# Optimization experiments

Hardware: AMD Instinct MI355X
Metric: run time of the kernel (lower is better)

Reference implementation:

```python
import jax, jax.numpy as jnp
import numpy as np

N = 50000  # num nodes


def _gcn_layer(x, W, b, src, dst, dinv):
    # PyG GCNConv: transform first, then normalized neighbor aggregation
    h = x @ W                                   # [N, out]
    norm = dinv[src] * dinv[dst]                # [E]
    msg = h[src] * norm[:, None]                # gather + scale, [E, out]
    agg = jax.ops.segment_sum(msg, dst, num_segments=N)
    agg = agg + h * (dinv * dinv)[:, None]      # self-loop term (weight 1)
    return agg + b


def setup_inputs() -> dict:
    key = jax.random.key(0)
    ks = jax.random.split(key, 9)
    x = jax.random.normal(ks[0], (N, 256), dtype=jnp.float32)
    edge_index = jax.random.randint(ks[1], (2, 800000), 0, N, dtype=jnp.int64)
    def lin(kw, kb, fan_in, fan_out):
        s = 1.0 / np.sqrt(fan_in)
        W = jax.random.uniform(kw, (fan_in, fan_out), jnp.float32, -s, s)
        b = jax.random.uniform(kb, (fan_out,), jnp.float32, -s, s)
        return W, b
    W0, b0 = lin(ks[2], ks[3], 256, 128)
    W1, b1 = lin(ks[4], ks[5], 128, 128)
    W2, b2 = lin(ks[6], ks[7], 128, 64)
    return {"x": x, "edge_index": edge_index,
            "W0": W0, "b0": b0, "W1": W1, "b1": b1, "W2": W2, "b2": b2}


def reference(x, edge_index, W0, b0, W1, b1, W2, b2):
    src, dst = edge_index[0], edge_index[1]
    # degree with implicit self loops (edge weights = 1)
    deg = jax.ops.segment_sum(jnp.ones_like(dst, dtype=x.dtype), dst,
                              num_segments=N) + 1.0
    dinv = jax.lax.rsqrt(deg)
    h = jax.nn.relu(_gcn_layer(x, W0, b0, src, dst, dinv))
    h = jax.nn.relu(_gcn_layer(h, W1, b1, src, dst, dinv))
    out = _gcn_layer(h, W2, b2, src, dst, dinv)  # no relu on final layer
    return out
```

## Files before the change

### kernel.cpp

```cpp
#include <hip/hip_runtime.h>

#define NNODES 50000
#define NEDGES 800000
#define CHUNK 3125

typedef __attribute__((ext_vector_type(8))) short short8;
typedef __attribute__((ext_vector_type(4))) float floatx4;
typedef __attribute__((ext_vector_type(8))) _Float16 f16x8;

__device__ __forceinline__ void async16(const void* g, void* l) {
    __builtin_amdgcn_global_load_lds(
        (const __attribute__((address_space(1))) unsigned int*)g,
        (__attribute__((address_space(3))) unsigned int*)l, 16, 0, 0);
}

__device__ __forceinline__ void split_bf16(float v, short& hi, short& lo) {
    unsigned u = __float_as_uint(v);
    unsigned hu = u & 0xffff0000u;
    hi = (short)(hu >> 16);
    float r = v - __uint_as_float(hu);
    lo = (short)(__float_as_uint(r) >> 16);
}


#define PREP_WBLK 224
#define PREP_SBLK 6250
#define PREP_TOT  (PREP_WBLK + PREP_SBLK + 256)

__global__ __launch_bounds__(256) void k_prep(
    const float* __restrict__ W0, short* __restrict__ W0h, short* __restrict__ W0l,
    const float* __restrict__ W1, short* __restrict__ W1h, short* __restrict__ W1l,
    const float* __restrict__ W2, short* __restrict__ W2h, short* __restrict__ W2l,
    const float* __restrict__ x, short* __restrict__ xh, short* __restrict__ xl,
    const int* __restrict__ dst, int* __restrict__ hist2d) {
    int b = blockIdx.x, t = threadIdx.x;
    if (b < PREP_WBLK) {
        int id = b * 256 + t;
        const float* W; short *Wh, *Wl; int K, F;
        if (id < 32768) { W = W0; Wh = W0h; Wl = W0l; K = 256; F = 128; }
        else if (id < 49152) { id -= 32768; W = W1; Wh = W1h; Wl = W1l; K = 128; F = 128; }
        else if (id < 57344) { id -= 49152; W = W2; Wh = W2h; Wl = W2l; K = 128; F = 64; }
        else return;
        int f = id / K, k = id - f * K;
        short h, l;
        split_bf16(W[(size_t)k * F + f], h, l);
        Wh[id] = h;
        Wl[id] = l;
    } else if (b < PREP_WBLK + PREP_SBLK) {
        int i = (b - PREP_WBLK) * 256 + t;
        float4 v0 = ((const float4*)x)[i * 2];
        float4 v1 = ((const float4*)x)[i * 2 + 1];
        float va[8] = {v0.x, v0.y, v0.z, v0.w, v1.x, v1.y, v1.z, v1.w};
        short8 h8, l8;
#pragma unroll
        for (int j = 0; j < 8; j++) {
            short h, l;
            split_bf16(va[j], h, l);
            h8[j] = h; l8[j] = l;
        }
        *(short8*)&xh[i * 8] = h8;
        *(short8*)&xl[i * 8] = l8;
    } else {
        __shared__ int h[256];
        int bb = b - PREP_WBLK - PREP_SBLK;
        h[t] = 0;
        __syncthreads();
        int e0 = bb * CHUNK;
#pragma unroll
        for (int k = 0; k < 13; k++) {
            int o = k * 256 + t;
            if (o < CHUNK) atomicAdd(&h[dst[e0 + o] >> 8], 1);
        }
        __syncthreads();
        hist2d[bb * 256 + t] = h[t];
    }
}

__global__ __launch_bounds__(256) void k_p2(const int* __restrict__ src,
                                            const int* __restrict__ dst,
                                            const int* __restrict__ hist2d,
                                            unsigned* __restrict__ buck) {
    __shared__ int ex[256], cur[256];
    int t = threadIdx.x, b = blockIdx.x;
    int tot = 0, pre = 0;
    for (int bb = 0; bb < 256; bb++) {
        int v = hist2d[bb * 256 + t];
        tot += v;
        pre += (bb < b) ? v : 0;
    }
    ex[t] = tot;
    __syncthreads();
    for (int o = 1; o < 256; o <<= 1) {
        int xx = (t >= o) ? ex[t - o] : 0;
        __syncthreads();
        ex[t] += xx;
        __syncthreads();
    }
    cur[t] = (ex[t] - tot) + pre;
    __syncthreads();
    int e0 = b * CHUNK;
#pragma unroll
    for (int k = 0; k < 13; k++) {
        int o = k * 256 + t;
        if (o < CHUNK) {
            int s = src[e0 + o], d = dst[e0 + o];
            int p = atomicAdd(&cur[d >> 8], 1);
            buck[p] = (unsigned)s | ((unsigned)(d & 255) << 16);
        }
    }
}

__global__ __launch_bounds__(256) void k_p3(const unsigned* __restrict__ buck,
                                            const int* __restrict__ hist2d,
                                            int* __restrict__ rowptr,
                                            float* __restrict__ dinv,
                                            int* __restrict__ ssrc) {
    __shared__ int ex[256], cur[256], h[256], sS0[1], sS[1];
    int t = threadIdx.x, b = blockIdx.x;
    int tot = 0;
    for (int bb = 0; bb < 256; bb++) tot += hist2d[bb * 256 + t];
    ex[t] = tot;
    __syncthreads();
    for (int o = 1; o < 256; o <<= 1) {
        int xx = (t >= o) ? ex[t - o] : 0;
        __syncthreads();
        ex[t] += xx;
        __syncthreads();
    }
    if (t == b) { sS0[0] = ex[t] - tot; sS[0] = tot; }
    h[t] = 0;
    __syncthreads();
    int s0 = sS0[0], S = sS[0];
    for (int i = t; i < S; i += 256)
        atomicAdd(&h[(buck[s0 + i] >> 16) & 255], 1);
    __syncthreads();
    int v = h[t];
    ex[t] = v;
    __syncthreads();
    for (int o = 1; o < 256; o <<= 1) {
        int xx = (t >= o) ? ex[t - o] : 0;
        __syncthreads();
        ex[t] += xx;
        __syncthreads();
    }
    int excl = ex[t] - v;
    int n = b * 256 + t;
    if (n < NNODES) {
        rowptr[n] = s0 + excl;
        dinv[n] = rsqrtf((float)v + 1.0f);
    }
    if (b == 0 && t == 0) rowptr[NNODES] = NEDGES;
    cur[t] = excl;
    __syncthreads();
    for (int i = t; i < S; i += 256) {
        unsigned pk = buck[s0 + i];
        int dl = (pk >> 16) & 255;
        int p = atomicAdd(&cur[dl], 1);
        ssrc[s0 + p] = (int)(pk & 0xFFFFu);
    }
}


template <int BN>
__global__ __launch_bounds__(256) void k_gemm2(
    const short* __restrict__ Ah, const short* __restrict__ Al,
    const short* __restrict__ Bh, const short* __restrict__ Bl,
    const float* __restrict__ dinv, _Float16* __restrict__ g16,
    int M, int K) {
    constexpr int BM = 64, BK = 64;
    constexpr int NT = BN / 16;
    __shared__ __align__(16) short sAh[BM * BK], sAl[BM * BK];
    __shared__ __align__(16) short sBh[BN * BK], sBl[BN * BK];

    const int tid = threadIdx.x, lane = tid & 63, w = tid >> 6;
    const int row0 = blockIdx.x * BM;
    const int lr = lane >> 3;
    const int lz = lane & 7;
    const int swz = (lz ^ lr) * 8;
    const int fr = lane & 15, fq = lane >> 4;

    floatx4 acc[NT] = {};

    for (int k0 = 0; k0 < K; k0 += BK) {
#pragma unroll
        for (int jj = 0; jj < 2; jj++) {
            int j = w * 2 + jj;
            int grow = row0 + j * 8 + lr;
            if (grow >= M) grow = M - 1;
            size_t go = (size_t)grow * K + k0 + swz;
            async16(&Ah[go], &sAh[j * 8 * BK + lane * 8]);
            async16(&Al[go], &sAl[j * 8 * BK + lane * 8]);
        }
#pragma unroll
        for (int jj = 0; jj < BN / 32; jj++) {
            int j = w * (BN / 32) + jj;
            size_t go = (size_t)(j * 8 + lr) * K + k0 + swz;
            async16(&Bh[go], &sBh[j * 8 * BK + lane * 8]);
            async16(&Bl[go], &sBl[j * 8 * BK + lane * 8]);
        }
        __syncthreads();

#pragma unroll
        for (int ks = 0; ks < 2; ks++) {
            int R = w * 16 + fr;
            int ca = ((ks * 4 + fq) ^ (R & 7)) * 8;
            short8 ah = *(const short8*)&sAh[R * BK + ca];
            short8 al = *(const short8*)&sAl[R * BK + ca];
#pragma unroll
            for (int nt = 0; nt < NT; nt++) {
                int n = nt * 16 + fr;
                int cb = ((ks * 4 + fq) ^ (n & 7)) * 8;
                short8 bh = *(const short8*)&sBh[n * BK + cb];
                short8 bl = *(const short8*)&sBl[n * BK + cb];
                acc[nt] = __builtin_amdgcn_mfma_f32_16x16x32_bf16(ah, bh, acc[nt], 0, 0, 0);
                acc[nt] = __builtin_amdgcn_mfma_f32_16x16x32_bf16(ah, bl, acc[nt], 0, 0, 0);
                acc[nt] = __builtin_amdgcn_mfma_f32_16x16x32_bf16(al, bh, acc[nt], 0, 0, 0);
            }
        }
        __syncthreads();
    }

#pragma unroll
    for (int rr = 0; rr < 4; rr++) {
        int grow = row0 + w * 16 + fq * 4 + rr;
        if (grow < M) {
            float dv = dinv[grow];
#pragma unroll
            for (int nt = 0; nt < NT; nt++)
                g16[(size_t)grow * BN + nt * 16 + fr] =
                    (_Float16)(acc[nt][rr] * dv);
        }
    }
}


template <int F>
__global__ __launch_bounds__(256) void k_agg(const _Float16* __restrict__ g,
                                             const int* __restrict__ ssrc,
                                             const int* __restrict__ rowptr,
                                             const float* __restrict__ dinv,
                                             const float* __restrict__ bias,
                                             float* __restrict__ outf,
                                             short* __restrict__ oh,
                                             short* __restrict__ ol,
                                             int relu, int writebf) {
    constexpr int F8 = F / 8;
    int gid = blockIdx.x * 256 + threadIdx.x;
    int n = gid / F8;
    if (n >= NNODES) return;
    int c8 = gid - n * F8;
    const f16x8* gp = (const f16x8*)g;

    f16x8 sv = gp[(size_t)n * F8 + c8];
    float a0[8], a1[8], a2[8], a3[8];
#pragma unroll
    for (int j = 0; j < 8; j++) {
        a0[j] = (float)sv[j];
        a1[j] = 0.f; a2[j] = 0.f; a3[j] = 0.f;
    }
    int e0 = rowptr[n], e1 = rowptr[n + 1];
    int e = e0;
    for (; e + 4 <= e1; e += 4) {
        int s0 = ssrc[e], s1 = ssrc[e + 1], s2 = ssrc[e + 2], s3 = ssrc[e + 3];
        f16x8 v0 = gp[(size_t)s0 * F8 + c8];
        f16x8 v1 = gp[(size_t)s1 * F8 + c8];
        f16x8 v2 = gp[(size_t)s2 * F8 + c8];
        f16x8 v3 = gp[(size_t)s3 * F8 + c8];
#pragma unroll
        for (int j = 0; j < 8; j++) {
            a0[j] += (float)v0[j];
            a1[j] += (float)v1[j];
            a2[j] += (float)v2[j];
            a3[j] += (float)v3[j];
        }
    }
    for (; e < e1; e++) {
        int s = ssrc[e];
        f16x8 v = gp[(size_t)s * F8 + c8];
#pragma unroll
        for (int j = 0; j < 8; j++) a0[j] += (float)v[j];
    }
    float dv = dinv[n];
    float o[8];
#pragma unroll
    for (int j = 0; j < 8; j++) {
        float s = (a0[j] + a1[j]) + (a2[j] + a3[j]);
        o[j] = s * dv + bias[c8 * 8 + j];
        if (relu) o[j] = fmaxf(o[j], 0.f);
    }
    if (writebf) {
        short8 h8, l8;
#pragma unroll
        for (int j = 0; j < 8; j++) {
            short h, l;
            split_bf16(o[j], h, l);
            h8[j] = h; l8[j] = l;
        }
        *(short8*)&oh[(size_t)n * F + c8 * 8] = h8;
        *(short8*)&ol[(size_t)n * F + c8 * 8] = l8;
    } else {
        *(float4*)&outf[(size_t)n * F + c8 * 8] =
            make_float4(o[0], o[1], o[2], o[3]);
        *(float4*)&outf[(size_t)n * F + c8 * 8 + 4] =
            make_float4(o[4], o[5], o[6], o[7]);
    }
}


static inline size_t align256(size_t x) { return (x + 255) & ~(size_t)255; }

extern "C" void kernel_launch(void* const* d_in, const int* in_sizes, int n_in,
                              void* d_out, int out_size, void* d_ws, size_t ws_size,
                              hipStream_t stream) {
    const float* x  = (const float*)d_in[0];
    const int*   ei = (const int*)d_in[1];
    const float* W0 = (const float*)d_in[2];
    const float* b0 = (const float*)d_in[3];
    const float* W1 = (const float*)d_in[4];
    const float* b1 = (const float*)d_in[5];
    const float* W2 = (const float*)d_in[6];
    const float* b2 = (const float*)d_in[7];
    float* out = (float*)d_out;

    const int* src = ei;
    const int* dst = ei + NEDGES;

    char* w = (char*)d_ws;
    size_t off = 0;
    float* dinv    = (float*)(w + off); off = align256(off + NNODES * 4);
    int* rowptr    = (int*)(w + off);   off = align256(off + (NNODES + 1) * 4);
    int* hist2d    = (int*)(w + off);   off = align256(off + 256 * 256 * 4);
    unsigned* buck = (unsigned*)(w + off); off = align256(off + (size_t)NEDGES * 4);
    int* ssrc      = (int*)(w + off);   off = align256(off + (size_t)NEDGES * 4);
    short* W0h     = (short*)(w + off); off = align256(off + 256 * 128 * 2);
    short* W0l     = (short*)(w + off); off = align256(off + 256 * 128 * 2);
    short* W1h     = (short*)(w + off); off = align256(off + 128 * 128 * 2);
    short* W1l     = (short*)(w + off); off = align256(off + 128 * 128 * 2);
    short* W2h     = (short*)(w + off); off = align256(off + 128 * 64 * 2);
    short* W2l     = (short*)(w + off); off = align256(off + 128 * 64 * 2);
    short* xh      = (short*)(w + off); off = align256(off + (size_t)NNODES * 256 * 2);
    short* xl      = (short*)(w + off); off = align256(off + (size_t)NNODES * 256 * 2);
    short* ph      = (short*)(w + off); off = align256(off + (size_t)NNODES * 128 * 2);
    short* pl      = (short*)(w + off); off = align256(off + (size_t)NNODES * 128 * 2);
    _Float16* g16  = (_Float16*)(w + off); off = align256(off + (size_t)NNODES * 128 * 2);

    k_prep<<<PREP_TOT, 256, 0, stream>>>(W0, W0h, W0l, W1, W1h, W1l,
                                         W2, W2h, W2l, x, xh, xl, dst, hist2d);
    k_p2<<<256, 256, 0, stream>>>(src, dst, hist2d, buck);
    k_p3<<<256, 256, 0, stream>>>(buck, hist2d, rowptr, dinv, ssrc);

    const int MB = (NNODES + 63) / 64;
    const int AB128 = (NNODES * 16 + 255) / 256;
    const int AB64  = (NNODES * 8 + 255) / 256;

    k_gemm2<128><<<MB, 256, 0, stream>>>(xh, xl, W0h, W0l, dinv, g16, NNODES, 256);
    k_agg<128><<<AB128, 256, 0, stream>>>(g16, ssrc, rowptr, dinv, b0,
                                          (float*)nullptr, ph, pl, 1, 1);
    k_gemm2<128><<<MB, 256, 0, stream>>>(ph, pl, W1h, W1l, dinv, g16, NNODES, 128);
    k_agg<128><<<AB128, 256, 0, stream>>>(g16, ssrc, rowptr, dinv, b1,
                                          (float*)nullptr, ph, pl, 1, 1);
    k_gemm2<64><<<MB, 256, 0, stream>>>(ph, pl, W2h, W2l, dinv, g16, NNODES, 128);
    k_agg<64><<<AB64, 256, 0, stream>>>(g16, ssrc, rowptr, dinv, b2,
                                        out, (short*)nullptr, (short*)nullptr, 0, 0);
    (void)in_sizes; (void)n_in; (void)out_size; (void)ws_size;
}
```

Before: 279.1 us.

## Fuse x bf16 split into first GEMM and fuse aggregation with next-layer GEMM

The separate pass that splits x into bf16 hi/lo arrays is removed; the first GEMM now reads fp32 x directly and splits it into LDS on the fly. Layers 1 and 2 fuse the neighbor aggregation (with bias, ReLU and hi/lo split) with the following layer's GEMM in one kernel, keeping the aggregated tile in LDS instead of writing and re-reading ph/pl from global memory. This cuts kernel launches and removes large intermediate global round trips. In exchange, the gather phase in the fused kernel runs with one 64-row block per 256 threads, which may lower memory-level parallelism for the irregular gathers.

```diff
diff --git a/kernel.cpp b/kernel.cpp
--- a/kernel.cpp
+++ b/kernel.cpp
@@ -24,14 +24,12 @@
 
 
 #define PREP_WBLK 224
-#define PREP_SBLK 6250
-#define PREP_TOT  (PREP_WBLK + PREP_SBLK + 256)
+#define PREP_TOT  (PREP_WBLK + 256)
 
 __global__ __launch_bounds__(256) void k_prep(
     const float* __restrict__ W0, short* __restrict__ W0h, short* __restrict__ W0l,
     const float* __restrict__ W1, short* __restrict__ W1h, short* __restrict__ W1l,
     const float* __restrict__ W2, short* __restrict__ W2h, short* __restrict__ W2l,
-    const float* __restrict__ x, short* __restrict__ xh, short* __restrict__ xl,
     const int* __restrict__ dst, int* __restrict__ hist2d) {
     int b = blockIdx.x, t = threadIdx.x;
     if (b < PREP_WBLK) {
@@ -46,23 +44,9 @@
         split_bf16(W[(size_t)k * F + f], h, l);
         Wh[id] = h;
         Wl[id] = l;
-    } else if (b < PREP_WBLK + PREP_SBLK) {
-        int i = (b - PREP_WBLK) * 256 + t;
-        float4 v0 = ((const float4*)x)[i * 2];
-        float4 v1 = ((const float4*)x)[i * 2 + 1];
-        float va[8] = {v0.x, v0.y, v0.z, v0.w, v1.x, v1.y, v1.z, v1.w};
-        short8 h8, l8;
-#pragma unroll
-        for (int j = 0; j < 8; j++) {
-            short h, l;
-            split_bf16(va[j], h, l);
-            h8[j] = h; l8[j] = l;
-        }
-        *(short8*)&xh[i * 8] = h8;
-        *(short8*)&xl[i * 8] = l8;
     } else {
         __shared__ int h[256];
-        int bb = b - PREP_WBLK - PREP_SBLK;
+        int bb = b - PREP_WBLK;
         h[t] = 0;
         __syncthreads();
         int e0 = bb * CHUNK;
@@ -161,57 +145,60 @@
 }
 
 
-template <int BN>
-__global__ __launch_bounds__(256) void k_gemm2(
-    const short* __restrict__ Ah, const short* __restrict__ Al,
-    const short* __restrict__ Bh, const short* __restrict__ Bl,
-    const float* __restrict__ dinv, _Float16* __restrict__ g16,
-    int M, int K) {
-    constexpr int BM = 64, BK = 64;
-    constexpr int NT = BN / 16;
-    __shared__ __align__(16) short sAh[BM * BK], sAl[BM * BK];
-    __shared__ __align__(16) short sBh[BN * BK], sBl[BN * BK];
-
-    const int tid = threadIdx.x, lane = tid & 63, w = tid >> 6;
-    const int row0 = blockIdx.x * BM;
-    const int lr = lane >> 3;
-    const int lz = lane & 7;
+__global__ __launch_bounds__(256) void k_gemm0(
+    const float* __restrict__ x, const short* __restrict__ Bh,
+    const short* __restrict__ Bl, const float* __restrict__ dinv,
+    _Float16* __restrict__ g16) {
+    __shared__ __align__(16) short sAh[64 * 64], sAl[64 * 64];
+    __shared__ __align__(16) short sBh[128 * 64], sBl[128 * 64];
+    const int t = threadIdx.x, lane = t & 63, w = t >> 6;
+    const int row0 = blockIdx.x * 64;
+    const int lr = lane >> 3, lz = lane & 7;
     const int swz = (lz ^ lr) * 8;
     const int fr = lane & 15, fq = lane >> 4;
-
-    floatx4 acc[NT] = {};
-
-    for (int k0 = 0; k0 < K; k0 += BK) {
-#pragma unroll
-        for (int jj = 0; jj < 2; jj++) {
-            int j = w * 2 + jj;
-            int grow = row0 + j * 8 + lr;
-            if (grow >= M) grow = M - 1;
-            size_t go = (size_t)grow * K + k0 + swz;
-            async16(&Ah[go], &sAh[j * 8 * BK + lane * 8]);
-            async16(&Al[go], &sAl[j * 8 * BK + lane * 8]);
-        }
-#pragma unroll
-        for (int jj = 0; jj < BN / 32; jj++) {
-            int j = w * (BN / 32) + jj;
-            size_t go = (size_t)(j * 8 + lr) * K + k0 + swz;
-            async16(&Bh[go], &sBh[j * 8 * BK + lane * 8]);
-            async16(&Bl[go], &sBl[j * 8 * BK + lane * 8]);
-        }
-        __syncthreads();
-
+    floatx4 acc[8] = {};
+    const int ar = t >> 2, ac = t & 3;
+    int garow = row0 + ar;
+    if (garow >= NNODES) garow = NNODES - 1;
+    const float* xrow = x + (size_t)garow * 256 + ac * 16;
+
+    for (int k0 = 0; k0 < 256; k0 += 64) {
+        const float4* xp = (const float4*)(xrow + k0);
+        float4 f0 = xp[0], f1 = xp[1], f2 = xp[2], f3 = xp[3];
+        float va[16] = {f0.x, f0.y, f0.z, f0.w, f1.x, f1.y, f1.z, f1.w,
+                        f2.x, f2.y, f2.z, f2.w, f3.x, f3.y, f3.z, f3.w};
+        short8 h0, h1, l0, l1;
+#pragma unroll
+        for (int j = 0; j < 8; j++) {
+            short h, l;
+            split_bf16(va[j], h, l);     h0[j] = h; l0[j] = l;
+            split_bf16(va[8 + j], h, l); h1[j] = h; l1[j] = l;
+        }
+        int c0 = ac * 2;
+        *(short8*)&sAh[ar * 64 + ((c0 ^ (ar & 7)) * 8)] = h0;
+        *(short8*)&sAh[ar * 64 + (((c0 + 1) ^ (ar & 7)) * 8)] = h1;
+        *(short8*)&sAl[ar * 64 + ((c0 ^ (ar & 7)) * 8)] = l0;
+        *(short8*)&sAl[ar * 64 + (((c0 + 1) ^ (ar & 7)) * 8)] = l1;
+#pragma unroll
+        for (int jj = 0; jj < 4; jj++) {
+            int j = w * 4 + jj;
+            size_t go = (size_t)(j * 8 + lr) * 256 + k0 + swz;
+            async16(&Bh[go], &sBh[j * 512 + lane * 8]);
+            async16(&Bl[go], &sBl[j * 512 + lane * 8]);
+        }
+        __syncthreads();
 #pragma unroll
         for (int ks = 0; ks < 2; ks++) {
             int R = w * 16 + fr;
             int ca = ((ks * 4 + fq) ^ (R & 7)) * 8;
-            short8 ah = *(const short8*)&sAh[R * BK + ca];
-            short8 al = *(const short8*)&sAl[R * BK + ca];
-#pragma unroll
-            for (int nt = 0; nt < NT; nt++) {
+            short8 ah = *(const short8*)&sAh[R * 64 + ca];
+            short8 al = *(const short8*)&sAl[R * 64 + ca];
+#pragma unroll
+            for (int nt = 0; nt < 8; nt++) {
                 int n = nt * 16 + fr;
                 int cb = ((ks * 4 + fq) ^ (n & 7)) * 8;
-                short8 bh = *(const short8*)&sBh[n * BK + cb];
-                short8 bl = *(const short8*)&sBl[n * BK + cb];
+                short8 bh = *(const short8*)&sBh[n * 64 + cb];
+                short8 bl = *(const short8*)&sBl[n * 64 + cb];
                 acc[nt] = __builtin_amdgcn_mfma_f32_16x16x32_bf16(ah, bh, acc[nt], 0, 0, 0);
                 acc[nt] = __builtin_amdgcn_mfma_f32_16x16x32_bf16(ah, bl, acc[nt], 0, 0, 0);
                 acc[nt] = __builtin_amdgcn_mfma_f32_16x16x32_bf16(al, bh, acc[nt], 0, 0, 0);
@@ -219,15 +206,122 @@
         }
         __syncthreads();
     }
-
 #pragma unroll
     for (int rr = 0; rr < 4; rr++) {
         int grow = row0 + w * 16 + fq * 4 + rr;
-        if (grow < M) {
+        if (grow < NNODES) {
             float dv = dinv[grow];
 #pragma unroll
+            for (int nt = 0; nt < 8; nt++)
+                g16[(size_t)grow * 128 + nt * 16 + fr] =
+                    (_Float16)(acc[nt][rr] * dv);
+        }
+    }
+}
+
+
+template <int BN>
+__global__ __launch_bounds__(256) void k_fg(
+    const _Float16* __restrict__ gin, const int* __restrict__ ssrc,
+    const int* __restrict__ rowptr, const float* __restrict__ dinv,
+    const float* __restrict__ bias, const short* __restrict__ Bh,
+    const short* __restrict__ Bl, _Float16* __restrict__ gout) {
+    constexpr int NT = BN / 16;
+    __shared__ __align__(16) short sAh[64 * 128], sAl[64 * 128];
+    __shared__ __align__(16) short sBh[BN * 32], sBl[BN * 32];
+    const int t = threadIdx.x, lane = t & 63, w = t >> 6;
+    const int row0 = blockIdx.x * 64;
+    const int fr = lane & 15, fq = lane >> 4;
+    const f16x8* gp = (const f16x8*)gin;
+
+    const int cc = t & 15;
+#pragma unroll
+    for (int pass = 0; pass < 4; pass++) {
+        int r = pass * 16 + (t >> 4);
+        int grow = row0 + r;
+        if (grow >= NNODES) grow = NNODES - 1;
+        f16x8 sv = gp[(size_t)grow * 16 + cc];
+        float a0[8], a1[8], a2[8], a3[8];
+#pragma unroll
+        for (int j = 0; j < 8; j++) {
+            a0[j] = (float)sv[j];
+            a1[j] = 0.f; a2[j] = 0.f; a3[j] = 0.f;
+        }
+        int e0 = rowptr[grow], e1 = rowptr[grow + 1];
+        int e = e0;
+        for (; e + 4 <= e1; e += 4) {
+            int s0 = ssrc[e], s1 = ssrc[e + 1], s2 = ssrc[e + 2], s3 = ssrc[e + 3];
+            f16x8 v0 = gp[(size_t)s0 * 16 + cc];
+            f16x8 v1 = gp[(size_t)s1 * 16 + cc];
+            f16x8 v2 = gp[(size_t)s2 * 16 + cc];
+            f16x8 v3 = gp[(size_t)s3 * 16 + cc];
+#pragma unroll
+            for (int j = 0; j < 8; j++) {
+                a0[j] += (float)v0[j];
+                a1[j] += (float)v1[j];
+                a2[j] += (float)v2[j];
+                a3[j] += (float)v3[j];
+            }
+        }
+        for (; e < e1; e++) {
+            int s = ssrc[e];
+            f16x8 v = gp[(size_t)s * 16 + cc];
+#pragma unroll
+            for (int j = 0; j < 8; j++) a0[j] += (float)v[j];
+        }
+        float dv = dinv[grow];
+        short8 h8, l8;
+#pragma unroll
+        for (int j = 0; j < 8; j++) {
+            float s = (a0[j] + a1[j]) + (a2[j] + a3[j]);
+            float o = fmaxf(s * dv + bias[cc * 8 + j], 0.f);
+            short hh, ll;
+            split_bf16(o, hh, ll);
+            h8[j] = hh; l8[j] = ll;
+        }
+        int slot = ((cc & 7) ^ (r & 7)) + (cc >> 3) * 8;
+        *(short8*)&sAh[r * 128 + slot * 8] = h8;
+        *(short8*)&sAl[r * 128 + slot * 8] = l8;
+    }
+    __syncthreads();
+
+    floatx4 acc[NT] = {};
+    const int lrB = lane >> 2, lzB = lane & 3;
+    for (int q = 0; q < 4; q++) {
+#pragma unroll
+        for (int jj = 0; jj < BN / 64; jj++) {
+            int j = w * (BN / 64) + jj;
+            int brow = j * 16 + lrB;
+            size_t go = (size_t)brow * 128 + q * 32 + ((lzB ^ (lrB & 3)) * 8);
+            async16(&Bh[go], &sBh[j * 512 + lane * 8]);
+            async16(&Bl[go], &sBl[j * 512 + lane * 8]);
+        }
+        __syncthreads();
+        int R = w * 16 + fr;
+        int c = q * 4 + fq;
+        int slotA = ((c & 7) ^ (R & 7)) + (c >> 3) * 8;
+        short8 ah = *(const short8*)&sAh[R * 128 + slotA * 8];
+        short8 al = *(const short8*)&sAl[R * 128 + slotA * 8];
+#pragma unroll
+        for (int nt = 0; nt < NT; nt++) {
+            int n = nt * 16 + fr;
+            short8 bh = *(const short8*)&sBh[n * 32 + ((fq ^ (n & 3)) * 8)];
+            short8 bl = *(const short8*)&sBl[n * 32 + ((fq ^ (n & 3)) * 8)];
+            acc[nt] = __builtin_amdgcn_mfma_f32_16x16x32_bf16(ah, bh, acc[nt], 0, 0, 0);
+            acc[nt] = __builtin_amdgcn_mfma_f32_16x16x32_bf16(ah, bl, acc[nt], 0, 0, 0);
+            acc[nt] = __builtin_amdgcn_mfma_f32_16x16x32_bf16(al, bh, acc[nt], 0, 0, 0);
+        }
+        __syncthreads();
+    }
+
+#pragma unroll
+    for (int rr = 0; rr < 4; rr++) {
+        int grow = row0 + w * 16 + fq * 4 + rr;
+        if (grow < NNODES) {
+            float dv = dinv[grow];
+#pragma unroll
             for (int nt = 0; nt < NT; nt++)
-                g16[(size_t)grow * BN + nt * 16 + fr] =
+                gout[(size_t)grow * BN + nt * 16 + fr] =
                     (_Float16)(acc[nt][rr] * dv);
         }
     }
@@ -240,10 +334,7 @@
                                              const int* __restrict__ rowptr,
                                              const float* __restrict__ dinv,
                                              const float* __restrict__ bias,
-                                             float* __restrict__ outf,
-                                             short* __restrict__ oh,
-                                             short* __restrict__ ol,
-                                             int relu, int writebf) {
+                                             float* __restrict__ outf) {
     constexpr int F8 = F / 8;
     int gid = blockIdx.x * 256 + threadIdx.x;
     int n = gid / F8;
@@ -286,24 +377,9 @@
     for (int j = 0; j < 8; j++) {
         float s = (a0[j] + a1[j]) + (a2[j] + a3[j]);
         o[j] = s * dv + bias[c8 * 8 + j];
-        if (relu) o[j] = fmaxf(o[j], 0.f);
-    }
-    if (writebf) {
-        short8 h8, l8;
-#pragma unroll
-        for (int j = 0; j < 8; j++) {
-            short h, l;
-            split_bf16(o[j], h, l);
-            h8[j] = h; l8[j] = l;
-        }
-        *(short8*)&oh[(size_t)n * F + c8 * 8] = h8;
-        *(short8*)&ol[(size_t)n * F + c8 * 8] = l8;
-    } else {
-        *(float4*)&outf[(size_t)n * F + c8 * 8] =
-            make_float4(o[0], o[1], o[2], o[3]);
-        *(float4*)&outf[(size_t)n * F + c8 * 8 + 4] =
-            make_float4(o[4], o[5], o[6], o[7]);
-    }
+    }
+    *(float4*)&outf[(size_t)n * F + c8 * 8] = make_float4(o[0], o[1], o[2], o[3]);
+    *(float4*)&outf[(size_t)n * F + c8 * 8 + 4] = make_float4(o[4], o[5], o[6], o[7]);
 }
 
 
@@ -338,29 +414,20 @@
     short* W1l     = (short*)(w + off); off = align256(off + 128 * 128 * 2);
     short* W2h     = (short*)(w + off); off = align256(off + 128 * 64 * 2);
     short* W2l     = (short*)(w + off); off = align256(off + 128 * 64 * 2);
-    short* xh      = (short*)(w + off); off = align256(off + (size_t)NNODES * 256 * 2);
-    short* xl      = (short*)(w + off); off = align256(off + (size_t)NNODES * 256 * 2);
-    short* ph      = (short*)(w + off); off = align256(off + (size_t)NNODES * 128 * 2);
-    short* pl      = (short*)(w + off); off = align256(off + (size_t)NNODES * 128 * 2);
-    _Float16* g16  = (_Float16*)(w + off); off = align256(off + (size_t)NNODES * 128 * 2);
+    _Float16* g16a = (_Float16*)(w + off); off = align256(off + (size_t)NNODES * 128 * 2);
+    _Float16* g16b = (_Float16*)(w + off); off = align256(off + (size_t)NNODES * 128 * 2);
+    _Float16* g16c = (_Float16*)(w + off); off = align256(off + (size_t)NNODES * 64 * 2);
+
+    const int MB = (NNODES + 63) / 64;
+    const int AB64 = (NNODES * 8 + 255) / 256;
 
     k_prep<<<PREP_TOT, 256, 0, stream>>>(W0, W0h, W0l, W1, W1h, W1l,
-                                         W2, W2h, W2l, x, xh, xl, dst, hist2d);
+                                         W2, W2h, W2l, dst, hist2d);
     k_p2<<<256, 256, 0, stream>>>(src, dst, hist2d, buck);
     k_p3<<<256, 256, 0, stream>>>(buck, hist2d, rowptr, dinv, ssrc);
-
-    const int MB = (NNODES + 63) / 64;
-    const int AB128 = (NNODES * 16 + 255) / 256;
-    const int AB64  = (NNODES * 8 + 255) / 256;
-
-    k_gemm2<128><<<MB, 256, 0, stream>>>(xh, xl, W0h, W0l, dinv, g16, NNODES, 256);
-    k_agg<128><<<AB128, 256, 0, stream>>>(g16, ssrc, rowptr, dinv, b0,
-                                          (float*)nullptr, ph, pl, 1, 1);
-    k_gemm2<128><<<MB, 256, 0, stream>>>(ph, pl, W1h, W1l, dinv, g16, NNODES, 128);
-    k_agg<128><<<AB128, 256, 0, stream>>>(g16, ssrc, rowptr, dinv, b1,
-                                          (float*)nullptr, ph, pl, 1, 1);
-    k_gemm2<64><<<MB, 256, 0, stream>>>(ph, pl, W2h, W2l, dinv, g16, NNODES, 128);
-    k_agg<64><<<AB64, 256, 0, stream>>>(g16, ssrc, rowptr, dinv, b2,
-                                        out, (short*)nullptr, (short*)nullptr, 0, 0);
+    k_gemm0<<<MB, 256, 0, stream>>>(x, W0h, W0l, dinv, g16a);
+    k_fg<128><<<MB, 256, 0, stream>>>(g16a, ssrc, rowptr, dinv, b0, W1h, W1l, g16b);
+    k_fg<64><<<MB, 256, 0, stream>>>(g16b, ssrc, rowptr, dinv, b1, W2h, W2l, g16c);
+    k_agg<64><<<AB64, 256, 0, stream>>>(g16c, ssrc, rowptr, dinv, b2, out);
     (void)in_sizes; (void)n_in; (void)out_size; (void)ws_size;
 }
```

Result: faster. 267.9 us (-4.0%).
